# Performance work log

Hardware: AMD Instinct MI355X
Metric: run time of the kernel (lower is better)

The kernel has to match this reference:

```python
import jax, jax.numpy as jnp
import numpy as np

B, S, E, H = 4, 2048, 1024, 16
D = E // H  # head dim = 64


def setup_inputs() -> dict:
    key = jax.random.key(0)
    ks = jax.random.split(key, 5)
    s = 0.02
    return {
        "x": jax.random.normal(ks[0], (B, S, E), dtype=jnp.float32),
        "Wq": jax.random.normal(ks[1], (E, E), dtype=jnp.float32) * s,
        "Wk": jax.random.normal(ks[2], (E, E), dtype=jnp.float32) * s,
        "Wv": jax.random.normal(ks[3], (E, E), dtype=jnp.float32) * s,
        "Wo": jax.random.normal(ks[4], (E, E), dtype=jnp.float32) * s,
        "bo": jnp.zeros((E,), dtype=jnp.float32),
    }


def reference(x, Wq, Wk, Wv, Wo, bo):
    b, s, e = x.shape
    h, d = H, e // H
    # QKV projections -> [b, h, s, d]
    q = (x @ Wq).reshape(b, s, h, d).transpose(0, 2, 1, 3)
    k = (x @ Wk).reshape(b, s, h, d).transpose(0, 2, 1, 3)
    v = (x @ Wv).reshape(b, s, h, d).transpose(0, 2, 1, 3)
    # scores [b, h, s, s], causal mask with -inf, scaled softmax
    a = jnp.einsum('bhqd,bhkd->bhqk', q, k)
    causal = jnp.tril(jnp.ones((s, s), dtype=bool))  # True where allowed
    a = jnp.where(causal, a, -jnp.inf) / jnp.sqrt(jnp.asarray(d, x.dtype))
    a = jax.nn.softmax(a, axis=-1)
    # dropout p=0.0 (identity in eval)
    y = jnp.einsum('bhqk,bhkd->bhqd', a, v)
    y = y.transpose(0, 2, 1, 3).reshape(b, s, e)
    return y @ Wo + bo
```

## Files before the change

kernel.cpp:

```cpp
#include <hip/hip_runtime.h>

typedef __bf16 bf16x8 __attribute__((ext_vector_type(8)));
typedef float f32x4 __attribute__((ext_vector_type(4)));
typedef unsigned short u16x8 __attribute__((ext_vector_type(8)));

#define S_LEN 2048
#define NHEAD 16
#define HDIM  64
#define EMB   1024

__device__ __forceinline__ ushort f2b(float v) {
  union { float f; unsigned u; } x; x.f = v;
  unsigned r = (x.u + 0x7fffu + ((x.u >> 16) & 1u)) >> 16;
  return (ushort)r;
}

__device__ __forceinline__ ushort f2b_trunc(float v) {
  union { float f; unsigned u; } x; x.f = v;
  return (ushort)(x.u >> 16);
}

typedef const __attribute__((address_space(1))) unsigned int* gp1_t;
typedef __attribute__((address_space(3))) unsigned int* lp3_t;
__device__ __forceinline__ void gld16(const ushort* g, const ushort* l) {
  __builtin_amdgcn_global_load_lds((gp1_t)(unsigned long long)(uintptr_t)g,
                                   (lp3_t)(unsigned int)(uintptr_t)l, 16, 0, 0);
}

__device__ __forceinline__ void barf() {
  asm volatile("" ::: "memory");
  __builtin_amdgcn_s_barrier();
  asm volatile("" ::: "memory");
}

__global__ __launch_bounds__(256) void prep_kernel(
    const float* __restrict__ x, const float* __restrict__ W0,
    const float* __restrict__ W1, const float* __restrict__ W2,
    const float* __restrict__ W3, ushort* __restrict__ xb,
    ushort* __restrict__ Wt0, ushort* __restrict__ Wt1,
    ushort* __restrict__ Wt2, ushort* __restrict__ Wt3, float scale0) {
  const int z = blockIdx.z;
  if (z == 4) {
    size_t base = ((size_t)(blockIdx.y * 32 + blockIdx.x)) * 8192 + threadIdx.x * 4;
#pragma unroll
    for (int i = 0; i < 8; ++i) {
      float4 v = *(const float4*)(x + base + i * 1024);
      ushort4 o;
      o.x = f2b(v.x); o.y = f2b(v.y); o.z = f2b(v.z); o.w = f2b(v.w);
      *(ushort4*)(xb + base + i * 1024) = o;
    }
    return;
  }
  __shared__ float t[32][33];
  const float* W = z == 0 ? W0 : (z == 1 ? W1 : (z == 2 ? W2 : W3));
  ushort* Wt = z == 0 ? Wt0 : (z == 1 ? Wt1 : (z == 2 ? Wt2 : Wt3));
  const float scale = z == 0 ? scale0 : 1.0f;
  int k0 = blockIdx.x * 32, n0 = blockIdx.y * 32;
  int c = threadIdx.x & 31, r0 = threadIdx.x >> 5;
#pragma unroll
  for (int i = 0; i < 4; ++i) {
    int r = r0 + i * 8;
    t[r][c] = W[(size_t)(k0 + r) * EMB + n0 + c];
  }
  __syncthreads();
#pragma unroll
  for (int i = 0; i < 4; ++i) {
    int r = r0 + i * 8;
    Wt[(size_t)(n0 + r) * EMB + k0 + c] = f2b(t[c][r] * scale);
  }
}

template <int EPI>
__global__ __launch_bounds__(512, 2) void gemm8_kernel(
    const ushort* __restrict__ A, const ushort* __restrict__ Bt,
    ushort* __restrict__ outQ, ushort* __restrict__ outK, ushort* __restrict__ outVt,
    float* __restrict__ outF, const float* __restrict__ bias) {
  __shared__ ushort lds8[49152];
  const int tid = threadIdx.x;
  const int wave = tid >> 6, lane = tid & 63, ln = lane & 15, quad = lane >> 4;
  const int wm = wave >> 2, wn = wave & 3;
  const long m0 = (long)blockIdx.x * 128, n0 = (long)blockIdx.y * 256;
  constexpr int K = EMB, KT = K / 64;

  const int srow = tid >> 2;
  const int scol = (tid & 3) * 8;
  const ushort* srcA  = A  + (m0 + srow) * (long)K + scol;
  const ushort* srcB0 = Bt + (n0 + srow) * (long)K + scol;
  const ushort* srcB1 = Bt + (n0 + 128 + srow) * (long)K + scol;
  const int dA_  = wave * 512;
  const int dB0_ = wave * 512;
  const int dB1_ = 4096 + wave * 512;

#define STG_A(kk, par, t)                                                      \
  gld16(srcA + (kk) * 32 + (t) * 64, lds8 + ((kk) * 2 + (par)) * 4096 + dA_)
#define STG_B(kk, par, t)                                                      \
  do {                                                                         \
    gld16(srcB0 + (kk) * 32 + (t) * 64,                                        \
          lds8 + 16384 + ((kk) * 2 + (par)) * 8192 + dB0_);                    \
    gld16(srcB1 + (kk) * 32 + (t) * 64,                                        \
          lds8 + 16384 + ((kk) * 2 + (par)) * 8192 + dB1_);                    \
  } while (0)

#define RD_A(kk, par)                                                          \
  do {                                                                         \
    const ushort* p_ = lds8 + ((kk) * 2 + (par)) * 4096 +                      \
                       (wm * 64 + ln) * 32 + quad * 8;                         \
    af[0] = *(const bf16x8*)p_;                                                \
    af[1] = *(const bf16x8*)(p_ + 512);                                        \
    af[2] = *(const bf16x8*)(p_ + 1024);                                       \
    af[3] = *(const bf16x8*)(p_ + 1536);                                       \
  } while (0)
#define RD_B(kk, par)                                                          \
  do {                                                                         \
    const ushort* p_ = lds8 + 16384 + ((kk) * 2 + (par)) * 8192 +              \
                       (wn * 64 + ln) * 32 + quad * 8;                         \
    bfr[0] = *(const bf16x8*)p_;                                               \
    bfr[1] = *(const bf16x8*)(p_ + 512);                                       \
    bfr[2] = *(const bf16x8*)(p_ + 1024);                                      \
    bfr[3] = *(const bf16x8*)(p_ + 1536);                                      \
  } while (0)

#define MM16()                                                                 \
  do {                                                                         \
    _Pragma("unroll") for (int mt = 0; mt < 4; ++mt)                           \
        _Pragma("unroll") for (int nt = 0; nt < 4; ++nt)                       \
            acc[mt][nt] = __builtin_amdgcn_mfma_f32_16x16x32_bf16(             \
                af[mt], bfr[nt], acc[mt][nt], 0, 0, 0);                        \
  } while (0)

  STG_A(0, 0, 0); STG_B(0, 0, 0);
  STG_A(1, 0, 0); STG_B(1, 0, 0);
  STG_A(0, 1, 1); STG_B(0, 1, 1);
  asm volatile("s_waitcnt vmcnt(3)" ::: "memory");
  barf();

  f32x4 acc[4][4] = {};
  bf16x8 af[4], bfr[4];

#define TILE(t, par, parn)                                                     \
  do {                                                                         \
                                                          \
    RD_A(0, par); RD_B(0, par);                                                \
    if ((t) + 1 < KT) { STG_A(1, parn, (t) + 1); STG_B(1, parn, (t) + 1); }    \
    barf();                                                                    \
    __builtin_amdgcn_s_setprio(1);                                             \
    MM16();                                                                    \
    __builtin_amdgcn_s_setprio(0);                                             \
    barf();                                                                    \
                                                          \
    RD_A(1, par); RD_B(1, par);                                                \
    if ((t) + 2 < KT) { STG_A(0, par, (t) + 2); STG_B(0, par, (t) + 2); }      \
    barf();                                                                    \
    __builtin_amdgcn_s_setprio(1);                                             \
    MM16();                                                                    \
    __builtin_amdgcn_s_setprio(0);                                             \
    if ((t) + 2 < KT) {                                                        \
      asm volatile("s_waitcnt vmcnt(3)" ::: "memory");                         \
    } else if ((t) + 1 < KT) {                                                 \
      asm volatile("s_waitcnt vmcnt(0)" ::: "memory");                         \
    }                                                                          \
    barf();                                                                    \
  } while (0)

  for (int th = 0; th < KT; th += 2) {
    TILE(th, 0, 1);
    TILE(th + 1, 1, 0);
  }

  if (EPI == 0) {
    const int sel = (int)(n0 >> 10);
    if (sel == 2) {
#pragma unroll
      for (int mt = 0; mt < 4; ++mt) {
        const long mbase = m0 + wm * 64 + mt * 16 + quad * 4;
        const long bb = mbase >> 11, s = mbase & 2047;
#pragma unroll
        for (int nt = 0; nt < 4; ++nt) {
          const int nn = (int)((n0 & 1023) + wn * 64 + nt * 16 + ln);
          const int h = nn >> 6, d = nn & 63;
          uint2 val;
          val.x = (unsigned)f2b(acc[mt][nt][0]) | ((unsigned)f2b(acc[mt][nt][1]) << 16);
          val.y = (unsigned)f2b(acc[mt][nt][2]) | ((unsigned)f2b(acc[mt][nt][3]) << 16);
          *(uint2*)(outVt + (((bb * NHEAD + h) * (long)HDIM + d) * S_LEN) + s) = val;
        }
      }
    } else {
      ushort* dst = sel == 0 ? outQ : outK;
#pragma unroll
      for (int mt = 0; mt < 4; ++mt) {
#pragma unroll
        for (int nt = 0; nt < 4; ++nt) {
          const int nn = (int)((n0 & 1023) + wn * 64 + nt * 16 + ln);
          const int h = nn >> 6, d = nn & 63;
#pragma unroll
          for (int r = 0; r < 4; ++r) {
            const long m = m0 + wm * 64 + mt * 16 + quad * 4 + r;
            const long bb = m >> 11, s = m & 2047;
            dst[(((bb * NHEAD + h) * S_LEN) + s) * HDIM + d] = f2b(acc[mt][nt][r]);
          }
        }
      }
    }
  } else {
#pragma unroll
    for (int mt = 0; mt < 4; ++mt) {
#pragma unroll
      for (int nt = 0; nt < 4; ++nt) {
        const long n = n0 + wn * 64 + nt * 16 + ln;
        const float bv = bias[n];
#pragma unroll
        for (int r = 0; r < 4; ++r) {
          const long m = m0 + wm * 64 + mt * 16 + quad * 4 + r;
          outF[m * (long)EMB + n] = acc[mt][nt][r] + bv;
        }
      }
    }
  }
#undef TILE
#undef MM16
#undef RD_B
#undef RD_A
#undef STG_B
#undef STG_A
}

__global__ __launch_bounds__(256) void attn_kernel(const ushort* __restrict__ Q,
                                                   const ushort* __restrict__ Kg,
                                                   const ushort* __restrict__ Vt,
                                                   ushort* __restrict__ Y) {
  __shared__ alignas(16) ushort Ks[2][2 * 64 * 32];
  __shared__ alignas(16) ushort Vs[2][2 * 64 * 32];
  __shared__ alignas(16) ushort Ps[4 * 2 * 16 * 72];
  const int tid = threadIdx.x;
  const int wave = tid >> 6, lane = tid & 63, ln = lane & 15, quad = lane >> 4;
  const int bh = blockIdx.x;
  const int qb = 15 - (int)blockIdx.y;
  const int q0 = qb * 128;
  const size_t base = (size_t)bh * S_LEN * HDIM;
  const int ntiles = 2 * qb + 2;

  const u16x8 ob = {0x3F80, 0x3F80, 0x3F80, 0x3F80, 0x3F80, 0x3F80, 0x3F80, 0x3F80};
  const bf16x8 ones = __builtin_bit_cast(bf16x8, ob);

  bf16x8 qf[2][2];
#pragma unroll
  for (int mt = 0; mt < 2; ++mt)
#pragma unroll
    for (int ks2 = 0; ks2 < 2; ++ks2)
      qf[mt][ks2] = *(const bf16x8*)(Q + base + (size_t)(q0 + wave * 32 + mt * 16 + ln) * HDIM +
                                     ks2 * 32 + quad * 8);

  f32x4 acc[2][4] = {};
  f32x4 accl[2] = {};

  const int sr = lane >> 2, sc = (lane & 3) * 8;
  const ushort* KgL = Kg + base + (size_t)(16 * wave + sr) * HDIM + sc;
  const ushort* VgL = Vt + base + (size_t)(16 * wave + sr) * S_LEN + sc;

  {
    ushort* kb = &Ks[0][16 * wave * 32];
    ushort* vb = &Vs[0][16 * wave * 32];
    gld16(KgL, kb);
    gld16(KgL + 32, kb + 2048);
    gld16(VgL, vb);
    gld16(VgL + 32, vb + 2048);
  }
  __syncthreads();

  ushort* Pw0 = Ps + wave * 2304;
  ushort* Pw1 = Pw0 + 1152;
  const int swW = (quad >> 1) << 4;
  const int swR = (ln >> 3) << 4;

  for (int kt = 0; kt < ntiles; ++kt) {
    const int cur = kt & 1;
    const int k0 = kt * 64;
    if (kt + 1 < ntiles) {
      const int nb = cur ^ 1;
      const size_t k1 = (size_t)(k0 + 64);
      ushort* kb = &Ks[nb][16 * wave * 32];
      ushort* vb = &Vs[nb][16 * wave * 32];
      gld16(KgL + k1 * HDIM, kb);
      gld16(KgL + k1 * HDIM + 32, kb + 2048);
      gld16(VgL + k1, vb);
      gld16(VgL + k1 + 32, vb + 2048);
    }
    const ushort* Kc = &Ks[cur][0];
    const ushort* Vc = &Vs[cur][0];
    const int qbase = q0 + wave * 32;

    if (k0 < qbase + 32) {
      f32x4 s0[4] = {}, s1[4] = {};
#pragma unroll
      for (int ks2 = 0; ks2 < 2; ++ks2) {
#pragma unroll
        for (int nt = 0; nt < 4; ++nt) {
          bf16x8 bk = *(const bf16x8*)(Kc + ks2 * 2048 + (nt * 16 + ln) * 32 + quad * 8);
          s0[nt] = __builtin_amdgcn_mfma_f32_16x16x32_bf16(qf[0][ks2], bk, s0[nt], 0, 0, 0);
          s1[nt] = __builtin_amdgcn_mfma_f32_16x16x32_bf16(qf[1][ks2], bk, s1[nt], 0, 0, 0);
        }
      }

      if (k0 + 63 > qbase) {
        const int rowq = qbase + quad * 4;
#pragma unroll
        for (int nt = 0; nt < 4; ++nt)
#pragma unroll
          for (int r = 0; r < 4; ++r) {
            const int key = k0 + nt * 16 + ln;
            if (key > rowq + r) s0[nt][r] = -3.0e38f;
            if (key > rowq + 16 + r) s1[nt][r] = -3.0e38f;
          }
      }

      asm volatile("" ::: "memory");
#pragma unroll
      for (int nt = 0; nt < 4; ++nt) {
#pragma unroll
        for (int r = 0; r < 4; ++r) {
          float p0 = __builtin_amdgcn_exp2f(s0[nt][r]);
          float p1 = __builtin_amdgcn_exp2f(s1[nt][r]);
          const int row = (quad * 4 + r) * 72;
          const int col = (nt * 16 + ln) ^ swW;
          Pw0[row + col] = f2b_trunc(p0);
          Pw1[row + col] = f2b_trunc(p1);
        }
      }
      asm volatile("" ::: "memory");

#pragma unroll
      for (int ks2 = 0; ks2 < 2; ++ks2) {
        const int rcol = (ks2 * 32 + quad * 8) ^ swR;
        bf16x8 ap0 = *(const bf16x8*)(Pw0 + ln * 72 + rcol);
        bf16x8 ap1 = *(const bf16x8*)(Pw1 + ln * 72 + rcol);
        accl[0] = __builtin_amdgcn_mfma_f32_16x16x32_bf16(ap0, ones, accl[0], 0, 0, 0);
        accl[1] = __builtin_amdgcn_mfma_f32_16x16x32_bf16(ap1, ones, accl[1], 0, 0, 0);
#pragma unroll
        for (int t2 = 0; t2 < 4; ++t2) {
          bf16x8 bv = *(const bf16x8*)(Vc + ks2 * 2048 + (t2 * 16 + ln) * 32 + quad * 8);
          acc[0][t2] = __builtin_amdgcn_mfma_f32_16x16x32_bf16(ap0, bv, acc[0][t2], 0, 0, 0);
          acc[1][t2] = __builtin_amdgcn_mfma_f32_16x16x32_bf16(ap1, bv, acc[1][t2], 0, 0, 0);
        }
      }
    }
    __syncthreads();
  }

  const long b = bh >> 4;
  const int h = bh & 15;
#pragma unroll
  for (int mt = 0; mt < 2; ++mt) {
#pragma unroll
    for (int r = 0; r < 4; ++r) {
      float inv = 1.0f / accl[mt][r];
      const int qq = q0 + wave * 32 + mt * 16 + quad * 4 + r;
#pragma unroll
      for (int t2 = 0; t2 < 4; ++t2)
        Y[(((b * S_LEN + qq) * NHEAD) + h) * HDIM + t2 * 16 + ln] = f2b(acc[mt][t2][r] * inv);
    }
  }
}

extern "C" void kernel_launch(void* const* d_in, const int* in_sizes, int n_in,
                              void* d_out, int out_size, void* d_ws, size_t ws_size,
                              hipStream_t stream) {
  const float* x  = (const float*)d_in[0];
  const float* Wq = (const float*)d_in[1];
  const float* Wk = (const float*)d_in[2];
  const float* Wv = (const float*)d_in[3];
  const float* Wo = (const float*)d_in[4];
  const float* bo = (const float*)d_in[5];
  float* out = (float*)d_out;

  const size_t XE = (size_t)8192 * EMB;
  ushort* ws    = (ushort*)d_ws;
  ushort* xb    = ws;
  ushort* Wtqkv = xb + XE;
  ushort* Wto   = Wtqkv + 3 * 1048576;
  ushort* Qb    = Wto + 1048576;
  ushort* Kb    = Qb + XE;
  ushort* Vtb   = Kb + XE;
  ushort* Yb    = xb;

  const float SCALE_Q = 1.4426950408889634f / 8.0f;

  prep_kernel<<<dim3(32, 32, 5), 256, 0, stream>>>(
      x, Wq, Wk, Wv, Wo, xb, Wtqkv, Wtqkv + 1048576, Wtqkv + 2097152, Wto, SCALE_Q);

  gemm8_kernel<0><<<dim3(64, 12), 512, 0, stream>>>(xb, Wtqkv, Qb, Kb, Vtb,
                                                    nullptr, nullptr);
  attn_kernel<<<dim3(64, 16), 256, 0, stream>>>(Qb, Kb, Vtb, Yb);
  gemm8_kernel<1><<<dim3(64, 4), 512, 0, stream>>>(Yb, Wto, nullptr, nullptr,
                                                   nullptr, out, bo);
}
```

Before: 242.9 us.

## Use three-stage LDS ring with XOR-swizzled full-K tiles in projection GEMM

Restructures the GEMM staging so each stage holds a full 64-wide K slice instead of two 32-wide halves. The buffers become a three-slot ring that prefetches two tiles ahead, and A/B loads are split across the two MMA phases. LDS rows are XOR-swizzled to avoid bank conflicts on the fragment reads. The aim is to hide global load latency better and cut LDS conflicts. The cost is that LDS per block grows to about 144KB, which likely limits the kernel to one 512-thread block per CU despite the launch bounds.

```diff
diff --git a/kernel.cpp b/kernel.cpp
--- a/kernel.cpp
+++ b/kernel.cpp
@@ -75,49 +75,50 @@
     const ushort* __restrict__ A, const ushort* __restrict__ Bt,
     ushort* __restrict__ outQ, ushort* __restrict__ outK, ushort* __restrict__ outVt,
     float* __restrict__ outF, const float* __restrict__ bias) {
-  __shared__ ushort lds8[49152];
+  __shared__ ushort lds8[73728];
   const int tid = threadIdx.x;
   const int wave = tid >> 6, lane = tid & 63, ln = lane & 15, quad = lane >> 4;
   const int wm = wave >> 2, wn = wave & 3;
   const long m0 = (long)blockIdx.x * 128, n0 = (long)blockIdx.y * 256;
   constexpr int K = EMB, KT = K / 64;
 
-  const int srow = tid >> 2;
-  const int scol = (tid & 3) * 8;
-  const ushort* srcA  = A  + (m0 + srow) * (long)K + scol;
-  const ushort* srcB0 = Bt + (n0 + srow) * (long)K + scol;
-  const ushort* srcB1 = Bt + (n0 + 128 + srow) * (long)K + scol;
-  const int dA_  = wave * 512;
-  const int dB0_ = wave * 512;
-  const int dB1_ = 4096 + wave * 512;
-
-#define STG_A(kk, par, t)                                                      \
-  gld16(srcA + (kk) * 32 + (t) * 64, lds8 + ((kk) * 2 + (par)) * 4096 + dA_)
-#define STG_B(kk, par, t)                                                      \
-  do {                                                                         \
-    gld16(srcB0 + (kk) * 32 + (t) * 64,                                        \
-          lds8 + 16384 + ((kk) * 2 + (par)) * 8192 + dB0_);                    \
-    gld16(srcB1 + (kk) * 32 + (t) * 64,                                        \
-          lds8 + 16384 + ((kk) * 2 + (par)) * 8192 + dB1_);                    \
-  } while (0)
-
-#define RD_A(kk, par)                                                          \
-  do {                                                                         \
-    const ushort* p_ = lds8 + ((kk) * 2 + (par)) * 4096 +                      \
-                       (wm * 64 + ln) * 32 + quad * 8;                         \
+  const int srow = tid >> 3;
+  const int scol = ((tid & 7) ^ (srow & 7)) * 8;
+  const ushort* srcA = A + (m0 + srow) * (long)K + scol;
+  const ushort* srcB = Bt + (n0 + srow) * (long)K + scol;
+
+#define STG_A(t, s)                                                            \
+  do {                                                                         \
+    gld16(srcA + (t) * 64,               lds8 + (s) * 8192 + tid * 8);         \
+    gld16(srcA + (t) * 64 + 64 * K,      lds8 + (s) * 8192 + 4096 + tid * 8);  \
+  } while (0)
+#define STG_B(t, s)                                                            \
+  do {                                                                         \
+    gld16(srcB + (t) * 64,               lds8 + 24576 + (s) * 16384 + tid * 8);         \
+    gld16(srcB + (t) * 64 + 64 * K,      lds8 + 24576 + (s) * 16384 + 4096 + tid * 8);  \
+    gld16(srcB + (t) * 64 + 128 * K,     lds8 + 24576 + (s) * 16384 + 8192 + tid * 8);  \
+    gld16(srcB + (t) * 64 + 192 * K,     lds8 + 24576 + (s) * 16384 + 12288 + tid * 8); \
+  } while (0)
+
+  const int sw = (ln & 7) * 8;
+
+#define RD_A(kk, s)                                                            \
+  do {                                                                         \
+    const ushort* p_ = lds8 + (s) * 8192 + (wm * 64 + ln) * 64 +               \
+                       (((kk) * 32 + quad * 8) ^ sw);                          \
     af[0] = *(const bf16x8*)p_;                                                \
-    af[1] = *(const bf16x8*)(p_ + 512);                                        \
-    af[2] = *(const bf16x8*)(p_ + 1024);                                       \
-    af[3] = *(const bf16x8*)(p_ + 1536);                                       \
-  } while (0)
-#define RD_B(kk, par)                                                          \
-  do {                                                                         \
-    const ushort* p_ = lds8 + 16384 + ((kk) * 2 + (par)) * 8192 +              \
-                       (wn * 64 + ln) * 32 + quad * 8;                         \
+    af[1] = *(const bf16x8*)(p_ + 1024);                                       \
+    af[2] = *(const bf16x8*)(p_ + 2048);                                       \
+    af[3] = *(const bf16x8*)(p_ + 3072);                                       \
+  } while (0)
+#define RD_B(kk, s)                                                            \
+  do {                                                                         \
+    const ushort* p_ = lds8 + 24576 + (s) * 16384 + (wn * 64 + ln) * 64 +      \
+                       (((kk) * 32 + quad * 8) ^ sw);                          \
     bfr[0] = *(const bf16x8*)p_;                                               \
-    bfr[1] = *(const bf16x8*)(p_ + 512);                                       \
-    bfr[2] = *(const bf16x8*)(p_ + 1024);                                      \
-    bfr[3] = *(const bf16x8*)(p_ + 1536);                                      \
+    bfr[1] = *(const bf16x8*)(p_ + 1024);                                      \
+    bfr[2] = *(const bf16x8*)(p_ + 2048);                                      \
+    bfr[3] = *(const bf16x8*)(p_ + 3072);                                      \
   } while (0)
 
 #define MM16()                                                                 \
@@ -128,44 +129,43 @@
                 af[mt], bfr[nt], acc[mt][nt], 0, 0, 0);                        \
   } while (0)
 
-  STG_A(0, 0, 0); STG_B(0, 0, 0);
-  STG_A(1, 0, 0); STG_B(1, 0, 0);
-  STG_A(0, 1, 1); STG_B(0, 1, 1);
-  asm volatile("s_waitcnt vmcnt(3)" ::: "memory");
+  STG_A(0, 0); STG_B(0, 0);
+  STG_A(1, 1); STG_B(1, 1);
+  asm volatile("s_waitcnt vmcnt(6)" ::: "memory");
   barf();
 
   f32x4 acc[4][4] = {};
   bf16x8 af[4], bfr[4];
 
-#define TILE(t, par, parn)                                                     \
-  do {                                                                         \
-                                                          \
-    RD_A(0, par); RD_B(0, par);                                                \
-    if ((t) + 1 < KT) { STG_A(1, parn, (t) + 1); STG_B(1, parn, (t) + 1); }    \
+#define TILE(t, s, sn)                                                         \
+  do {                                                                         \
+    RD_A(0, s); RD_B(0, s);                                                    \
+    if ((t) + 2 < KT) STG_A((t) + 2, sn);                                      \
     barf();                                                                    \
     __builtin_amdgcn_s_setprio(1);                                             \
     MM16();                                                                    \
     __builtin_amdgcn_s_setprio(0);                                             \
     barf();                                                                    \
-                                                          \
-    RD_A(1, par); RD_B(1, par);                                                \
-    if ((t) + 2 < KT) { STG_A(0, par, (t) + 2); STG_B(0, par, (t) + 2); }      \
+    RD_A(1, s); RD_B(1, s);                                                    \
+    if ((t) + 2 < KT) STG_B((t) + 2, sn);                                      \
     barf();                                                                    \
     __builtin_amdgcn_s_setprio(1);                                             \
     MM16();                                                                    \
     __builtin_amdgcn_s_setprio(0);                                             \
     if ((t) + 2 < KT) {                                                        \
-      asm volatile("s_waitcnt vmcnt(3)" ::: "memory");                         \
+      asm volatile("s_waitcnt vmcnt(6)" ::: "memory");                         \
     } else if ((t) + 1 < KT) {                                                 \
       asm volatile("s_waitcnt vmcnt(0)" ::: "memory");                         \
     }                                                                          \
     barf();                                                                    \
   } while (0)
 
-  for (int th = 0; th < KT; th += 2) {
-    TILE(th, 0, 1);
+  for (int th = 0; th < 15; th += 3) {
+    TILE(th, 0, 2);
     TILE(th + 1, 1, 0);
-  }
+    TILE(th + 2, 2, 1);
+  }
+  TILE(15, 0, 2);
 
   if (EPI == 0) {
     const int sel = (int)(n0 >> 10);
```

Result: faster. 230.6 us (-5.1%).
